# Optimization experiments

Hardware: AMD Instinct MI355X
Metric: run time of the kernel (lower is better)

Reference implementation:

```python
import jax, jax.numpy as jnp
import numpy as np

HID = 1024
HEADS = 16
HEAD_DIM = HID // HEADS
NEG = -10000000000.0


def setup_inputs() -> dict:
    key = jax.random.key(0)
    ks = jax.random.split(key, 12)
    B, S = 4, 2048
    scale = 1.0 / np.sqrt(HID)
    inp = {
        "query": jax.random.normal(ks[0], (B, S, HID), dtype=jnp.float32),
        "key": jax.random.normal(ks[1], (B, S, HID), dtype=jnp.float32),
        "value": jax.random.normal(ks[2], (B, S, HID), dtype=jnp.float32),
        "Wq": jax.random.normal(ks[3], (HID, HID), dtype=jnp.float32) * scale,
        "bq": jnp.zeros((HID,), dtype=jnp.float32),
        "Wk": jax.random.normal(ks[4], (HID, HID), dtype=jnp.float32) * scale,
        "bk": jnp.zeros((HID,), dtype=jnp.float32),
        "Wv": jax.random.normal(ks[5], (HID, HID), dtype=jnp.float32) * scale,
        "bv": jnp.zeros((HID,), dtype=jnp.float32),
        "Wo": jax.random.normal(ks[6], (HID, HID), dtype=jnp.float32) * scale,
        "bo": jnp.zeros((HID,), dtype=jnp.float32),
    }
    return inp


def reference(query, key, value, Wq, bq, Wk, bk, Wv, bv, Wo, bo):
    B, S, _ = query.shape
    # linear projections (nn.Linear: x @ W.T + b)
    q = query @ Wq.T + bq
    k = key @ Wk.T + bk
    v = value @ Wv.T + bv
    # split heads -> [B, H, S, D]
    q = q.reshape(B, S, HEADS, HEAD_DIM).transpose(0, 2, 1, 3)
    k = k.reshape(B, S, HEADS, HEAD_DIM).transpose(0, 2, 1, 3)
    v = v.reshape(B, S, HEADS, HEAD_DIM).transpose(0, 2, 1, 3)
    # NOTE: original module computes self.scale but never applies it -> unscaled logits
    attn = jnp.einsum("bhqd,bhkd->bhqk", q, k)
    causal = jnp.tril(jnp.ones((S, S), dtype=bool))
    attn = jnp.where(causal, attn, NEG)
    attn = jax.nn.softmax(attn, axis=-1)
    x = jnp.einsum("bhqk,bhkd->bhqd", attn, v)
    x = x.transpose(0, 2, 1, 3).reshape(B, S, HID)
    return x @ Wo.T + bo
```

## Files before the change

### kernel.cpp

```cpp
#include <hip/hip_runtime.h>
#include <hip/hip_fp16.h>

typedef _Float16 half_t;
typedef half_t halfx8 __attribute__((ext_vector_type(8)));
typedef half_t halfx4 __attribute__((ext_vector_type(4)));
typedef float floatx4 __attribute__((ext_vector_type(4)));

#define HID 1024
#define HEADS 16
#define HD 64
#define BATCH 4
#define SEQ 2048
#define MTOT (BATCH * SEQ)
#define NWELEM (HID * HID)

#define MFMA_F16 __builtin_amdgcn_mfma_f32_16x16x32_f16

__device__ inline halfx8 load8h(const half_t* p) { return *(const halfx8*)p; }
__device__ inline halfx8 load8h(const float* p) {
    floatx4 x = *(const floatx4*)p;
    floatx4 y = *(const floatx4*)(p + 4);
    halfx8 r;
    r[0] = (half_t)x[0]; r[1] = (half_t)x[1];
    r[2] = (half_t)x[2]; r[3] = (half_t)x[3];
    r[4] = (half_t)y[0]; r[5] = (half_t)y[1];
    r[6] = (half_t)y[2]; r[7] = (half_t)y[3];
    return r;
}

__device__ __forceinline__ uint32_t pack2h(float a, float b) {
    union { half_t h[2]; uint32_t u; } r;
    r.h[0] = (half_t)a; r.h[1] = (half_t)b;
    return r.u;
}

__device__ __forceinline__ void gl_lds16(const half_t* g, half_t* lds) {
    __builtin_amdgcn_global_load_lds(
        (const __attribute__((address_space(1))) void*)g,
        (__attribute__((address_space(3))) void*)lds, 16, 0, 0);
}

template <int MODE, typename TOut>
__device__ __forceinline__ void epilogue_store(
    const floatx4 (&acc)[4][4], const float* __restrict__ bias,
    TOut* __restrict__ Out, int m0, int n0, int wm, int wn, int quad, int l16)
{
    float bvals[4];
#pragma unroll
    for (int nt = 0; nt < 4; ++nt)
        bvals[nt] = bias[n0 + wn + nt * 16 + l16];

#pragma unroll
    for (int mt = 0; mt < 4; ++mt) {
        const int mbase = m0 + wm + mt * 16 + quad * 4;
#pragma unroll
        for (int nt = 0; nt < 4; ++nt) {
            const int n = n0 + wn + nt * 16 + l16;
            if (MODE == 2) {
                const int b = mbase >> 11, s = mbase & (SEQ - 1);
                const int h = n >> 6, d = n & (HD - 1);
                halfx4 st;
#pragma unroll
                for (int r = 0; r < 4; ++r)
                    st[r] = (half_t)(acc[mt][nt][r] + bvals[nt]);
                *(halfx4*)((half_t*)Out +
                    ((((size_t)b * HEADS + h) * HD + d) << 11) + s) = st;
            } else {
#pragma unroll
                for (int r = 0; r < 4; ++r) {
                    const float v = acc[mt][nt][r] + bvals[nt];
                    const int mm  = mbase + r;
                    if (MODE == 0) {
                        const int b = mm >> 11, s = mm & (SEQ - 1);
                        const int h = n >> 6, d = n & (HD - 1);
                        Out[((((size_t)b * HEADS + h) * SEQ + s) << 6) + d] = (TOut)v;
                    } else {
                        Out[(size_t)mm * HID + n] = (TOut)v;
                    }
                }
            }
        }
    }
}

template <int MODE, typename TOut>
__global__ __launch_bounds__(256) void gemm16(
    const half_t* __restrict__ A, const half_t* __restrict__ W,
    const float* __restrict__ bias, TOut* __restrict__ Out)
{
    __shared__ half_t As[128 * 32];
    __shared__ half_t Bs[128 * 32];

    const int tid  = threadIdx.x;
    const int id   = blockIdx.y * gridDim.x + blockIdx.x;
    const int cpx  = (gridDim.x * gridDim.y) >> 3;
    const int swz  = (id & 7) * cpx + (id >> 3);
    const int m0   = (swz >> 3) * 128;
    const int n0   = (swz & 7) * 128;
    const int wave = tid >> 6;
    const int lane = tid & 63;
    const int quad = lane >> 4;
    const int l16  = lane & 15;
    const int wm   = (wave >> 1) * 64;
    const int wn   = (wave & 1) * 64;

    const int c0   = wave * 2;
    const int srow = c0 * 16 + (lane >> 2);
    const int scol = (lane & 3) * 8;
    const half_t* aptr0 = A + (size_t)(m0 + srow) * HID + scol;
    const half_t* aptr1 = aptr0 + (size_t)16 * HID;
    const half_t* bptr0 = W + (size_t)(n0 + srow) * HID + scol;
    const half_t* bptr1 = bptr0 + (size_t)16 * HID;
    half_t* ldsA0 = &As[c0 * 512];
    half_t* ldsA1 = &As[c0 * 512 + 512];
    half_t* ldsB0 = &Bs[c0 * 512];
    half_t* ldsB1 = &Bs[c0 * 512 + 512];

    floatx4 acc[4][4];
    const floatx4 zero4 = {0.f, 0.f, 0.f, 0.f};
#pragma unroll
    for (int mt = 0; mt < 4; ++mt)
#pragma unroll
        for (int nt = 0; nt < 4; ++nt) acc[mt][nt] = zero4;

    for (int k0 = 0; k0 < HID; k0 += 32) {
        __syncthreads();
        gl_lds16(aptr0 + k0, ldsA0);
        gl_lds16(aptr1 + k0, ldsA1);
        gl_lds16(bptr0 + k0, ldsB0);
        gl_lds16(bptr1 + k0, ldsB1);
        __syncthreads();

        halfx8 af[4], bfr[4];
#pragma unroll
        for (int t = 0; t < 4; ++t) {
            af[t]  = *(const halfx8*)&As[(wm + t * 16 + l16) * 32 + quad * 8];
            bfr[t] = *(const halfx8*)&Bs[(wn + t * 16 + l16) * 32 + quad * 8];
        }
#pragma unroll
        for (int mt = 0; mt < 4; ++mt)
#pragma unroll
            for (int nt = 0; nt < 4; ++nt)
                acc[mt][nt] = MFMA_F16(af[mt], bfr[nt], acc[mt][nt], 0, 0, 0);
    }

    epilogue_store<MODE, TOut>(acc, bias, Out, m0, n0, wm, wn, quad, l16);
}

template <int MODE, typename TA, typename TOut>
__global__ __launch_bounds__(256) void gemm_bt(
    const TA* __restrict__ A, const float* __restrict__ W,
    const float* __restrict__ bias, TOut* __restrict__ Out)
{
    __shared__ half_t As[128][40];
    __shared__ half_t Bs[128][40];

    const int tid  = threadIdx.x;
    const int m0   = blockIdx.y * 128;
    const int n0   = blockIdx.x * 128;
    const int wave = tid >> 6;
    const int lane = tid & 63;
    const int quad = lane >> 4;
    const int l16  = lane & 15;
    const int wm   = (wave >> 1) * 64;
    const int wn   = (wave & 1) * 64;
    const int trow = tid >> 1;
    const int tcol = (tid & 1) * 16;

    const TA*    aptr = A + (size_t)(m0 + trow) * HID + tcol;
    const float* bptr = W + (size_t)(n0 + trow) * HID + tcol;

    floatx4 acc[4][4];
    const floatx4 zero4 = {0.f, 0.f, 0.f, 0.f};
#pragma unroll
    for (int mt = 0; mt < 4; ++mt)
#pragma unroll
        for (int nt = 0; nt < 4; ++nt) acc[mt][nt] = zero4;

    for (int k0 = 0; k0 < HID; k0 += 32) {
        halfx8 av0 = load8h(aptr);
        halfx8 av1 = load8h(aptr + 8);
        halfx8 bv0 = load8h(bptr);
        halfx8 bv1 = load8h(bptr + 8);
        aptr += 32;
        bptr += 32;

        __syncthreads();
        *(halfx8*)&As[trow][tcol]     = av0;
        *(halfx8*)&As[trow][tcol + 8] = av1;
        *(halfx8*)&Bs[trow][tcol]     = bv0;
        *(halfx8*)&Bs[trow][tcol + 8] = bv1;
        __syncthreads();

        halfx8 af[4], bfr[4];
#pragma unroll
        for (int t = 0; t < 4; ++t) {
            af[t]  = *(const halfx8*)&As[wm + t * 16 + l16][quad * 8];
            bfr[t] = *(const halfx8*)&Bs[wn + t * 16 + l16][quad * 8];
        }
#pragma unroll
        for (int mt = 0; mt < 4; ++mt)
#pragma unroll
            for (int nt = 0; nt < 4; ++nt)
                acc[mt][nt] = MFMA_F16(af[mt], bfr[nt], acc[mt][nt], 0, 0, 0);
    }

    epilogue_store<MODE, TOut>(acc, bias, Out, m0, n0, wm, wn, quad, l16);
}

__global__ __launch_bounds__(256) void cvt_act(
    const float* __restrict__ in, half_t* __restrict__ out)
{
    const size_t i = ((size_t)blockIdx.x * 256 + threadIdx.x) * 8;
    *(halfx8*)(out + i) = load8h(in + i);
}

__global__ __launch_bounds__(256) void cvt_w4(
    const float* __restrict__ w0, const float* __restrict__ w1,
    const float* __restrict__ w2, const float* __restrict__ w3,
    half_t* __restrict__ out)
{
    const int t = blockIdx.y;
    const float* src = (t == 0) ? w0 : (t == 1) ? w1 : (t == 2) ? w2 : w3;
    const size_t i = ((size_t)blockIdx.x * 256 + threadIdx.x) * 8;
    *(halfx8*)(out + (size_t)t * NWELEM + i) = load8h(src + i);
}

__global__ __launch_bounds__(256) void attn_kernel(
    const half_t* __restrict__ Q, const half_t* __restrict__ K,
    const half_t* __restrict__ VT, half_t* __restrict__ O)
{
    __shared__ half_t Ks[64][72];
    __shared__ half_t Vt[64][72];

    const int bh  = blockIdx.x;
    const int qt  = (gridDim.y - 1) - blockIdx.y;
    const int q0  = qt * 128;
    const int tid = threadIdx.x;
    const int wave = tid >> 6;
    const int lane = tid & 63;
    const int quad = lane >> 4;
    const int l16  = lane & 15;

    const half_t* Qb  = Q  + (size_t)bh * SEQ * HD;
    const half_t* Kb  = K  + (size_t)bh * SEQ * HD;
    const half_t* VTb = VT + (size_t)bh * HD * SEQ;

    halfx8 aq[2][2];
#pragma unroll
    for (int mt = 0; mt < 2; ++mt) {
        const half_t* p = Qb + (size_t)(q0 + wave * 32 + mt * 16 + l16) * HD + quad * 8;
        aq[mt][0] = *(const halfx8*)p;
        aq[mt][1] = *(const halfx8*)(p + 32);
    }

    const floatx4 zero4 = {0.f, 0.f, 0.f, 0.f};
    floatx4 oaccT[2][4];
    float mrow[2], lrow[2];
#pragma unroll
    for (int mt = 0; mt < 2; ++mt) {
        mrow[mt] = -3.0e38f;
        lrow[mt] = 0.f;
#pragma unroll
        for (int dt = 0; dt < 4; ++dt) oaccT[mt][dt] = zero4;
    }

    const int srow = tid >> 2;
    const int scol = (tid & 3) * 16;
    const int ktiles = 2 * qt + 2;

    union U8 { halfx8 h; uint32_t u[4]; };

    for (int kt = 0; kt < ktiles; ++kt) {
        const int k0 = kt * 64;
        __syncthreads();
        {
            const half_t* ksrc = Kb + (size_t)(k0 + srow) * HD + scol;
            *(halfx8*)&Ks[srow][scol]     = *(const halfx8*)ksrc;
            *(halfx8*)&Ks[srow][scol + 8] = *(const halfx8*)(ksrc + 8);
            const half_t* vsrc = VTb + (size_t)srow * SEQ + k0 + scol;
            *(halfx8*)&Vt[srow][scol]     = *(const halfx8*)vsrc;
            *(halfx8*)&Vt[srow][scol + 8] = *(const halfx8*)(vsrc + 8);
        }
        __syncthreads();

        const bool active = (k0 <= q0 + wave * 32 + 31);

        if (active) {
            floatx4 sacc[2][4];
#pragma unroll
            for (int mt = 0; mt < 2; ++mt)
#pragma unroll
                for (int nt = 0; nt < 4; ++nt) sacc[mt][nt] = zero4;
#pragma unroll
            for (int nt = 0; nt < 4; ++nt) {
                halfx8 bk0 = *(const halfx8*)&Ks[nt * 16 + l16][quad * 8];
                halfx8 bk1 = *(const halfx8*)&Ks[nt * 16 + l16][quad * 8 + 32];
#pragma unroll
                for (int mt = 0; mt < 2; ++mt) {
                    sacc[mt][nt] = MFMA_F16(bk0, aq[mt][0], sacc[mt][nt], 0, 0, 0);
                    sacc[mt][nt] = MFMA_F16(bk1, aq[mt][1], sacc[mt][nt], 0, 0, 0);
                }
            }

            if (kt >= 2 * qt) {
#pragma unroll
                for (int mt = 0; mt < 2; ++mt) {
                    const int qg = q0 + wave * 32 + mt * 16 + l16;
#pragma unroll
                    for (int nt = 0; nt < 4; ++nt) {
                        const int kg = k0 + nt * 16 + quad * 4;
#pragma unroll
                        for (int r = 0; r < 4; ++r)
                            if (kg + r > qg) sacc[mt][nt][r] = -1.0e30f;
                    }
                }
            }

            uint32_t pk[2][4][2];
#pragma unroll
            for (int mt = 0; mt < 2; ++mt) {
                float mx = sacc[mt][0][0];
#pragma unroll
                for (int nt = 0; nt < 4; ++nt)
#pragma unroll
                    for (int r = 0; r < 4; ++r)
                        if (nt | r) mx = fmaxf(mx, sacc[mt][nt][r]);
                mx = fmaxf(mx, __shfl_xor(mx, 16));
                mx = fmaxf(mx, __shfl_xor(mx, 32));
                const float mnew  = fmaxf(mrow[mt], mx);
                const float alpha = __expf(mrow[mt] - mnew);
                mrow[mt] = mnew;

                float rsum = 0.f;
#pragma unroll
                for (int nt = 0; nt < 4; ++nt)
#pragma unroll
                    for (int r = 0; r < 4; ++r) {
                        const float p = __expf(sacc[mt][nt][r] - mnew);
                        sacc[mt][nt][r] = p;
                        rsum += p;
                    }
#pragma unroll
                for (int nt = 0; nt < 4; ++nt) {
                    pk[mt][nt][0] = pack2h(sacc[mt][nt][0], sacc[mt][nt][1]);
                    pk[mt][nt][1] = pack2h(sacc[mt][nt][2], sacc[mt][nt][3]);
                }
                rsum += __shfl_xor(rsum, 16);
                rsum += __shfl_xor(rsum, 32);
                lrow[mt] = lrow[mt] * alpha + rsum;
#pragma unroll
                for (int dt = 0; dt < 4; ++dt) oaccT[mt][dt] *= alpha;
            }

            U8 pb[2][2];
#pragma unroll
            for (int mt = 0; mt < 2; ++mt)
#pragma unroll
                for (int s2 = 0; s2 < 2; ++s2)
#pragma unroll
                    for (int w = 0; w < 4; ++w) {
                        const int src = l16 + ((quad & 1) << 5) + ((w >> 1) << 4);
                        const uint32_t lo =
                            (uint32_t)__shfl((int)pk[mt][2 * s2][w & 1], src, 64);
                        const uint32_t hi =
                            (uint32_t)__shfl((int)pk[mt][2 * s2 + 1][w & 1], src, 64);
                        pb[mt][s2].u[w] = (quad >> 1) ? hi : lo;
                    }

#pragma unroll
            for (int s2 = 0; s2 < 2; ++s2)
#pragma unroll
                for (int dt = 0; dt < 4; ++dt) {
                    halfx8 bv = *(const halfx8*)&Vt[dt * 16 + l16][s2 * 32 + quad * 8];
                    oaccT[0][dt] = MFMA_F16(bv, pb[0][s2].h, oaccT[0][dt], 0, 0, 0);
                    oaccT[1][dt] = MFMA_F16(bv, pb[1][s2].h, oaccT[1][dt], 0, 0, 0);
                }
        }
    }

    const int b = bh >> 4, h = bh & (HEADS - 1);
#pragma unroll
    for (int mt = 0; mt < 2; ++mt) {
        const int q = q0 + wave * 32 + mt * 16 + l16;
#pragma unroll
        for (int dt = 0; dt < 4; ++dt) {
            halfx4 st;
#pragma unroll
            for (int r = 0; r < 4; ++r)
                st[r] = (half_t)(oaccT[mt][dt][r] / lrow[mt]);
            *(halfx4*)(O + (size_t)(b * SEQ + q) * HID +
                       h * HD + dt * 16 + quad * 4) = st;
        }
    }
}

extern "C" void kernel_launch(void* const* d_in, const int* in_sizes, int n_in,
                              void* d_out, int out_size, void* d_ws, size_t ws_size,
                              hipStream_t stream)
{
    const float* query = (const float*)d_in[0];
    const float* key   = (const float*)d_in[1];
    const float* value = (const float*)d_in[2];
    const float* Wq    = (const float*)d_in[3];
    const float* bq    = (const float*)d_in[4];
    const float* Wk    = (const float*)d_in[5];
    const float* bk    = (const float*)d_in[6];
    const float* Wv    = (const float*)d_in[7];
    const float* bv    = (const float*)d_in[8];
    const float* Wo    = (const float*)d_in[9];
    const float* bo    = (const float*)d_in[10];
    float* out = (float*)d_out;

    const size_t NE = (size_t)MTOT * HID;
    half_t* Qp  = (half_t*)d_ws;
    half_t* Kp  = Qp  + NE;
    half_t* VpT = Kp  + NE;
    half_t* Ob  = VpT + NE;
    half_t* W16 = Ob  + NE;
    const size_t need = (4 * NE + 4 * (size_t)NWELEM) * sizeof(half_t);

    dim3 gg(HID / 128, MTOT / 128);
    dim3 ga(BATCH * HEADS, SEQ / 128);

    if (ws_size >= need) {
        half_t* act16 = Ob;
        const unsigned actBlocks = (unsigned)(NE / 2048);
        const unsigned wBlocks   = (unsigned)(NWELEM / 2048);

        cvt_w4<<<dim3(wBlocks, 4), 256, 0, stream>>>(Wq, Wk, Wv, Wo, W16);

        cvt_act<<<actBlocks, 256, 0, stream>>>(query, act16);
        gemm16<0, half_t><<<gg, 256, 0, stream>>>(act16, W16, bq, Qp);
        cvt_act<<<actBlocks, 256, 0, stream>>>(key, act16);
        gemm16<0, half_t><<<gg, 256, 0, stream>>>(act16, W16 + NWELEM, bk, Kp);
        cvt_act<<<actBlocks, 256, 0, stream>>>(value, act16);
        gemm16<2, half_t><<<gg, 256, 0, stream>>>(act16, W16 + 2 * (size_t)NWELEM, bv, VpT);

        attn_kernel<<<ga, 256, 0, stream>>>(Qp, Kp, VpT, Ob);

        gemm16<1, float><<<gg, 256, 0, stream>>>(Ob, W16 + 3 * (size_t)NWELEM, bo, out);
    } else {
        gemm_bt<0, float, half_t><<<gg, 256, 0, stream>>>(query, Wq, bq, Qp);
        gemm_bt<0, float, half_t><<<gg, 256, 0, stream>>>(key,   Wk, bk, Kp);
        gemm_bt<2, float, half_t><<<gg, 256, 0, stream>>>(value, Wv, bv, VpT);
        attn_kernel<<<ga, 256, 0, stream>>>(Qp, Kp, VpT, Ob);
        gemm_bt<1, half_t, float><<<gg, 256, 0, stream>>>(Ob, Wo, bo, out);
    }
}
```

Measured before the change: 362.1 us.

## Double-buffer GEMM LDS tiles, prefetch attention K/V, lazy softmax rescale

The fp16 GEMM now uses two LDS buffers so the next K-slice's global-to-LDS copy is issued before computing on the current one, which halves the barriers per k-step. The attention kernel prefetches the next K/V tile into registers while computing the current tile. The online softmax skips the rescale of the running max, sum and output when the new block max stays within 8 of the old max, saving exps and multiplies. The risks are higher LDS and register use, and exp values up to e^8 held in fp16 P, which could hurt accuracy.

```diff
diff --git a/kernel.cpp b/kernel.cpp
--- a/kernel.cpp
+++ b/kernel.cpp
@@ -88,8 +88,8 @@
     const half_t* __restrict__ A, const half_t* __restrict__ W,
     const float* __restrict__ bias, TOut* __restrict__ Out)
 {
-    __shared__ half_t As[128 * 32];
-    __shared__ half_t Bs[128 * 32];
+    __shared__ half_t As[2][128 * 32];
+    __shared__ half_t Bs[2][128 * 32];
 
     const int tid  = threadIdx.x;
     const int id   = blockIdx.y * gridDim.x + blockIdx.x;
@@ -111,10 +111,6 @@
     const half_t* aptr1 = aptr0 + (size_t)16 * HID;
     const half_t* bptr0 = W + (size_t)(n0 + srow) * HID + scol;
     const half_t* bptr1 = bptr0 + (size_t)16 * HID;
-    half_t* ldsA0 = &As[c0 * 512];
-    half_t* ldsA1 = &As[c0 * 512 + 512];
-    half_t* ldsB0 = &Bs[c0 * 512];
-    half_t* ldsB1 = &Bs[c0 * 512 + 512];
 
     floatx4 acc[4][4];
     const floatx4 zero4 = {0.f, 0.f, 0.f, 0.f};
@@ -123,25 +119,35 @@
 #pragma unroll
         for (int nt = 0; nt < 4; ++nt) acc[mt][nt] = zero4;
 
-    for (int k0 = 0; k0 < HID; k0 += 32) {
-        __syncthreads();
-        gl_lds16(aptr0 + k0, ldsA0);
-        gl_lds16(aptr1 + k0, ldsA1);
-        gl_lds16(bptr0 + k0, ldsB0);
-        gl_lds16(bptr1 + k0, ldsB1);
-        __syncthreads();
-
+    auto stage = [&](int buf, int k0) {
+        gl_lds16(aptr0 + k0, &As[buf][c0 * 512]);
+        gl_lds16(aptr1 + k0, &As[buf][c0 * 512 + 512]);
+        gl_lds16(bptr0 + k0, &Bs[buf][c0 * 512]);
+        gl_lds16(bptr1 + k0, &Bs[buf][c0 * 512 + 512]);
+    };
+    auto compute = [&](int buf) {
         halfx8 af[4], bfr[4];
 #pragma unroll
         for (int t = 0; t < 4; ++t) {
-            af[t]  = *(const halfx8*)&As[(wm + t * 16 + l16) * 32 + quad * 8];
-            bfr[t] = *(const halfx8*)&Bs[(wn + t * 16 + l16) * 32 + quad * 8];
+            af[t]  = *(const halfx8*)&As[buf][(wm + t * 16 + l16) * 32 + quad * 8];
+            bfr[t] = *(const halfx8*)&Bs[buf][(wn + t * 16 + l16) * 32 + quad * 8];
         }
 #pragma unroll
         for (int mt = 0; mt < 4; ++mt)
 #pragma unroll
             for (int nt = 0; nt < 4; ++nt)
                 acc[mt][nt] = MFMA_F16(af[mt], bfr[nt], acc[mt][nt], 0, 0, 0);
+    };
+
+    stage(0, 0);
+    __syncthreads();
+    for (int k0 = 0; k0 < HID; k0 += 64) {
+        stage(1, k0 + 32);
+        compute(0);
+        __syncthreads();
+        if (k0 + 64 < HID) stage(0, k0 + 64);
+        compute(1);
+        __syncthreads();
     }
 
     epilogue_store<MODE, TOut>(acc, bias, Out, m0, n0, wm, wn, quad, l16);
@@ -271,18 +277,34 @@
 
     union U8 { halfx8 h; uint32_t u[4]; };
 
+    halfx8 nk0, nk1, nv0, nv1;
+    {
+        const half_t* ksrc = Kb + (size_t)srow * HD + scol;
+        nk0 = *(const halfx8*)ksrc;
+        nk1 = *(const halfx8*)(ksrc + 8);
+        const half_t* vsrc = VTb + (size_t)srow * SEQ + scol;
+        nv0 = *(const halfx8*)vsrc;
+        nv1 = *(const halfx8*)(vsrc + 8);
+    }
+
     for (int kt = 0; kt < ktiles; ++kt) {
         const int k0 = kt * 64;
         __syncthreads();
-        {
-            const half_t* ksrc = Kb + (size_t)(k0 + srow) * HD + scol;
-            *(halfx8*)&Ks[srow][scol]     = *(const halfx8*)ksrc;
-            *(halfx8*)&Ks[srow][scol + 8] = *(const halfx8*)(ksrc + 8);
-            const half_t* vsrc = VTb + (size_t)srow * SEQ + k0 + scol;
-            *(halfx8*)&Vt[srow][scol]     = *(const halfx8*)vsrc;
-            *(halfx8*)&Vt[srow][scol + 8] = *(const halfx8*)(vsrc + 8);
-        }
-        __syncthreads();
+        *(halfx8*)&Ks[srow][scol]     = nk0;
+        *(halfx8*)&Ks[srow][scol + 8] = nk1;
+        *(halfx8*)&Vt[srow][scol]     = nv0;
+        *(halfx8*)&Vt[srow][scol + 8] = nv1;
+        __syncthreads();
+
+        if (kt + 1 < ktiles) {
+            const int kn = k0 + 64;
+            const half_t* ksrc = Kb + (size_t)(kn + srow) * HD + scol;
+            nk0 = *(const halfx8*)ksrc;
+            nk1 = *(const halfx8*)(ksrc + 8);
+            const half_t* vsrc = VTb + (size_t)srow * SEQ + kn + scol;
+            nv0 = *(const halfx8*)vsrc;
+            nv1 = *(const halfx8*)(vsrc + 8);
+        }
 
         const bool active = (k0 <= q0 + wave * 32 + 31);
 
@@ -328,16 +350,22 @@
                         if (nt | r) mx = fmaxf(mx, sacc[mt][nt][r]);
                 mx = fmaxf(mx, __shfl_xor(mx, 16));
                 mx = fmaxf(mx, __shfl_xor(mx, 32));
-                const float mnew  = fmaxf(mrow[mt], mx);
-                const float alpha = __expf(mrow[mt] - mnew);
-                mrow[mt] = mnew;
+
+                if (!__all(mx <= mrow[mt] + 8.f)) {
+                    const float mnew  = fmaxf(mrow[mt], mx);
+                    const float alpha = __expf(mrow[mt] - mnew);
+                    mrow[mt] = mnew;
+                    lrow[mt] *= alpha;
+#pragma unroll
+                    for (int dt = 0; dt < 4; ++dt) oaccT[mt][dt] *= alpha;
+                }
 
                 float rsum = 0.f;
 #pragma unroll
                 for (int nt = 0; nt < 4; ++nt)
 #pragma unroll
                     for (int r = 0; r < 4; ++r) {
-                        const float p = __expf(sacc[mt][nt][r] - mnew);
+                        const float p = __expf(sacc[mt][nt][r] - mrow[mt]);
                         sacc[mt][nt][r] = p;
                         rsum += p;
                     }
@@ -348,9 +376,7 @@
                 }
                 rsum += __shfl_xor(rsum, 16);
                 rsum += __shfl_xor(rsum, 32);
-                lrow[mt] = lrow[mt] * alpha + rsum;
-#pragma unroll
-                for (int dt = 0; dt < 4; ++dt) oaccT[mt][dt] *= alpha;
+                lrow[mt] += rsum;
             }
 
             U8 pb[2][2];
```

New measurement: 364.9 us. About the same (+0.8%).
